# Optimization experiments

Hardware: AMD Instinct MI355X
Metric: run time of the kernel (lower is better)

## Reference

```python
import jax, jax.numpy as jnp
import numpy as np

N = 6            # fixed by nn.Linear(6, h2) after the transpose/squeeze
NEG_SLOPE = 0.01 # F.leaky_relu default


def setup_inputs() -> dict:
    key = jax.random.key(0)
    ks = jax.random.split(key, 12)
    B, H1, H2, H3 = 131072, 64, 512, 256
    in_feat = jax.random.normal(ks[0], (N, B, 1), dtype=jnp.float32)
    # deterministic bidirectional ring: every node has in/out degree 2 (norm='both' safe)
    ar = jnp.arange(N, dtype=jnp.int32)
    src = jnp.concatenate([ar, ar])
    dst = jnp.concatenate([(ar + 1) % N, (ar - 1) % N]).astype(jnp.int32)
    s = 0.2
    W0  = jax.random.normal(ks[1], (1, H1), jnp.float32) * s
    b0  = jax.random.normal(ks[2], (H1,), jnp.float32) * s
    W1  = jax.random.normal(ks[3], (H1, 1), jnp.float32) * s
    b1  = jax.random.normal(ks[4], (1,), jnp.float32) * s
    Wl0 = jax.random.normal(ks[5], (N, H2), jnp.float32) * s
    bl0 = jax.random.normal(ks[6], (H2,), jnp.float32) * s
    Wl2 = jax.random.normal(ks[7], (H2, H3), jnp.float32) * s
    bl2 = jax.random.normal(ks[8], (H3,), jnp.float32) * s
    Wl3 = jax.random.normal(ks[9], (H3, 1), jnp.float32) * s
    bl3 = jax.random.normal(ks[10], (1,), jnp.float32) * s
    return {"in_feat": in_feat, "src": src, "dst": dst,
            "W0": W0, "b0": b0, "W1": W1, "b1": b1,
            "Wl0": Wl0, "bl0": bl0, "Wl2": Wl2, "bl2": bl2,
            "Wl3": Wl3, "bl3": bl3}


def _lrelu(x):
    return jnp.where(x >= 0, x, NEG_SLOPE * x)


def _degree_norms(src, dst):
    ones = jnp.ones(src.shape[0], dtype=jnp.float32)
    deg_out = jax.ops.segment_sum(ones, src, num_segments=N)
    deg_in = jax.ops.segment_sum(ones, dst, num_segments=N)
    return deg_out ** -0.5, deg_in ** -0.5  # DGL GraphConv norm='both'


def _graph_conv(feat, W, b, src, dst, inv_out, inv_in):
    # D_out^{-1/2} A^T D_in^{-1/2} feat  then linear (order is math-equivalent)
    h = feat * inv_out[:, None, None]           # [N,B,F]
    agg = jax.ops.segment_sum(h[src], dst, num_segments=N)  # gather+scatter over edges
    agg = agg * inv_in[:, None, None]
    return agg @ W + b


def reference(in_feat, src, dst, W0, b0, W1, b1, Wl0, bl0, Wl2, bl2, Wl3, bl3):
    inv_out, inv_in = _degree_norms(src, dst)
    h = _lrelu(_graph_conv(in_feat, W0, b0, src, dst, inv_out, inv_in))  # [N,B,h1]
    h = _lrelu(_graph_conv(h, W1, b1, src, dst, inv_out, inv_in))        # [N,B,1]
    x = jnp.transpose(h, (2, 1, 0))[0]   # transpose(0,2).squeeze(0) -> [B,N]
    x = _lrelu(x @ Wl0 + bl0)
    x = _lrelu(x @ Wl2 + bl2)
    x = _lrelu(x @ Wl3 + bl3)            # [B,1]; squeeze(0) is a no-op for B>1
    return x
```

## Files before the change

kernel.cpp:

```cpp
#include <hip/hip_runtime.h>

#define NN   6
#define H1   64
#define H2   512
#define H3   256
#define TM   256
#define KC   32
#define NCH  (H2 / KC)
#define CHUNK_BYTES 32768

typedef short s16x8 __attribute__((ext_vector_type(8)));
typedef float f32x16 __attribute__((ext_vector_type(16)));
typedef float f32x2 __attribute__((ext_vector_type(2)));
typedef unsigned int u32x4 __attribute__((ext_vector_type(4)));

__device__ __forceinline__ unsigned short f2bf(float x) {
    unsigned int u = __float_as_uint(x);
    u += 0x7FFFu + ((u >> 16) & 1u);
    return (unsigned short)(u >> 16);
}
__device__ __forceinline__ float bf2f(unsigned short b) {
    return __uint_as_float(((unsigned int)b) << 16);
}
__device__ __forceinline__ unsigned int cvt_pk_bf16(float a, float b) {
    unsigned int r;
    asm("v_cvt_pk_bf16_f32 %0, %1, %2" : "=v"(r) : "v"(a), "v"(b));
    return r;
}
__device__ __forceinline__ void g2lds16(const void* g, void* l) {
    __builtin_amdgcn_global_load_lds(
        (const __attribute__((address_space(1))) unsigned int*)g,
        (__attribute__((address_space(3))) unsigned int*)l, 16, 0, 0);
}

__global__ void split_w(const float* __restrict__ Wl2,
                        unsigned short* __restrict__ Whl) {
    const int tid = blockIdx.x * 256 + threadIdx.x;
    const int c0 = tid >> 13, q = tid & 8191;
    const int j = q & 7, col = (q >> 3) & 255, th = q >> 11;
    const int k = (c0 << 5) + (th << 3) + j;
    const float w = Wl2[k * H3 + col];
    const unsigned short hi = f2bf(w);
    const unsigned short lo = f2bf(w - bf2f(hi));
    Whl[(c0 << 14) + q] = hi;
    Whl[(c0 << 14) + 8192 + q] = lo;
}

__global__ __launch_bounds__(512, 2)
void gcn_mfma(const float* __restrict__ f,
              const float* __restrict__ W0,
              const float* __restrict__ b0,
              const float* __restrict__ W1,
              const float* __restrict__ b1_,
              const float* __restrict__ Wl0,
              const float* __restrict__ bl0,
              const float* __restrict__ bl2,
              const float* __restrict__ Wl3,
              const float* __restrict__ bl3_,
              const unsigned short* __restrict__ Whl,
              float* __restrict__ out,
              int B)
{
    __shared__ float sW0[H1], sB0[H1], sW1[H1];
    __shared__ float sWl0[NN][H2];
    __shared__ float sBl0[H2];
    __shared__ float sBl2[H3];
    __shared__ float sWl3[H3];
    __shared__ float sF[NN][TM];
    __shared__ float sS[NN][TM];
    __shared__ float sX[NN][TM];
    __shared__ __align__(16) unsigned short sB[2][16384];

    const int t    = threadIdx.x;
    const int lane = t & 63;
    const int w    = t >> 6;
    const int cl   = lane & 31;
    const int h    = lane >> 5;
    const int m0   = blockIdx.x * TM;

    for (int i = t; i < H1; i += 512) { sW0[i] = W0[i]; sB0[i] = b0[i]; sW1[i] = W1[i]; }
    for (int i = t; i < NN * H2; i += 512) sWl0[i >> 9][i & (H2 - 1)] = Wl0[i];
    for (int i = t; i < H2; i += 512) sBl0[i] = bl0[i];
    for (int i = t; i < H3; i += 512) { sBl2[i] = bl2[i]; sWl3[i] = Wl3[i]; }
    for (int i = t; i < NN * TM; i += 512) sF[i >> 8][i & 255] = f[(i >> 8) * B + m0 + (i & 255)];

#define STAGE(CH, BUF) do {                                                        \
        const char* _src = (const char*)Whl + (CH) * CHUNK_BYTES + (w << 12) + (lane << 4); \
        char*       _dst = (char*)&sB[BUF][0] + (w << 12);                         \
        _Pragma("unroll")                                                          \
        for (int _q = 0; _q < 4; ++_q) g2lds16(_src + (_q << 10), _dst + (_q << 10)); \
    } while (0)

    STAGE(0, 0);
    __syncthreads();

    const float b1v = b1_[0];

    for (int v = t; v < NN * TM; v += 512) {
        const int i = v >> 8, r = v & 255;
        const int im = (i + NN - 1) % NN, ip = (i + 1) % NN;
        const float g = 0.5f * (sF[im][r] + sF[ip][r]);
        float s = 0.f;
        #pragma unroll
        for (int c = 0; c < H1; ++c) {
            float hx = g * sW0[c] + sB0[c];
            hx = fmaxf(hx, 0.01f * hx);
            s += hx * sW1[c];
        }
        sS[i][r] = s;
    }
    __syncthreads();
    for (int v = t; v < NN * TM; v += 512) {
        const int i = v >> 8, r = v & 255;
        const int im = (i + NN - 1) % NN, ip = (i + 1) % NN;
        const float xv = 0.5f * (sS[im][r] + sS[ip][r]) + b1v;
        sX[i][r] = fmaxf(xv, 0.01f * xv);
    }
    __syncthreads();

    const int myrow = (w << 5) + cl;
    float xr[NN];
    #pragma unroll
    for (int i = 0; i < NN; ++i) xr[i] = sX[i][myrow];

    f32x16 acc[8];
    #pragma unroll
    for (int c = 0; c < 8; ++c)
        #pragma unroll
        for (int rg = 0; rg < 16; ++rg) acc[c][rg] = 0.f;

#define K0(CH, TT) (((CH) << 5) + ((TT) << 4) + (h << 3))
#define GEN_TT(K0V, AH, AL) do {                                                   \
        const int _k0 = (K0V);                                                     \
        f32x2 _ac[4];                                                              \
        _Pragma("unroll")                                                          \
        for (int _j = 0; _j < 4; ++_j) _ac[_j] = *(const f32x2*)&sBl0[_k0 + 2*_j]; \
        _Pragma("unroll")                                                          \
        for (int _i = 0; _i < 6; ++_i) {                                           \
            const float _xi = xr[_i];                                              \
            _Pragma("unroll")                                                      \
            for (int _j = 0; _j < 4; ++_j)                                         \
                _ac[_j] += _xi * (*(const f32x2*)&sWl0[_i][_k0 + 2*_j]);           \
        }                                                                          \
        unsigned int _hw[4], _lw[4];                                               \
        _Pragma("unroll")                                                          \
        for (int _j = 0; _j < 4; ++_j) {                                           \
            f32x2 _v = _ac[_j];                                                    \
            _v = __builtin_elementwise_max(_v, 0.01f * _v);                        \
            const unsigned int _uh = cvt_pk_bf16(_v[0], _v[1]);                    \
            f32x2 _hf = { __uint_as_float(_uh << 16),                              \
                          __uint_as_float(_uh & 0xFFFF0000u) };                    \
            const f32x2 _r = _v - _hf;                                             \
            _hw[_j] = _uh; _lw[_j] = cvt_pk_bf16(_r[0], _r[1]);                    \
        }                                                                          \
        const u32x4 _u4 = {_hw[0], _hw[1], _hw[2], _hw[3]};                        \
        const u32x4 _l4 = {_lw[0], _lw[1], _lw[2], _lw[3]};                        \
        AH = __builtin_bit_cast(s16x8, _u4);                                       \
        AL = __builtin_bit_cast(s16x8, _l4);                                       \
    } while (0)

#define MFMA_TT(SBC, TT, AH, AL) do {                                              \
        const int _thh = ((TT) << 1) + h;                                          \
        const unsigned short* _bb = &(SBC)[((_thh << 8) + cl) << 3];               \
        _Pragma("unroll")                                                          \
        for (int _g = 0; _g < 2; ++_g) {                                           \
            s16x8 _bh[4];                                                          \
            _Pragma("unroll")                                                      \
            for (int _i = 0; _i < 4; ++_i)                                         \
                _bh[_i] = *(const s16x8*)&_bb[(_g * 4 + _i) << 8];                 \
            _Pragma("unroll")                                                      \
            for (int _i = 0; _i < 4; ++_i)                                         \
                acc[_g*4+_i] = __builtin_amdgcn_mfma_f32_32x32x16_bf16(AH, _bh[_i], acc[_g*4+_i], 0, 0, 0); \
            _Pragma("unroll")                                                      \
            for (int _i = 0; _i < 4; ++_i)                                         \
                acc[_g*4+_i] = __builtin_amdgcn_mfma_f32_32x32x16_bf16(AL, _bh[_i], acc[_g*4+_i], 0, 0, 0); \
            _Pragma("unroll")                                                      \
            for (int _i = 0; _i < 4; ++_i) {                                       \
                const s16x8 _bl = *(const s16x8*)&_bb[8192 + ((_g * 4 + _i) << 8)];\
                acc[_g*4+_i] = __builtin_amdgcn_mfma_f32_32x32x16_bf16(AH, _bl, acc[_g*4+_i], 0, 0, 0); \
            }                                                                      \
        }                                                                          \
    } while (0)

    s16x8 ahA0, alA0, ahA1, alA1;
    s16x8 ahB0, alB0, ahB1, alB1;
    GEN_TT(K0(0, 0), ahA0, alA0);
    GEN_TT(K0(0, 1), ahA1, alA1);

    for (int ch = 0; ch < NCH; ch += 2) {
        STAGE(ch + 1, 1);
        GEN_TT(K0(ch + 1, 0), ahB0, alB0);
        GEN_TT(K0(ch + 1, 1), ahB1, alB1);
        MFMA_TT((&sB[0][0]), 0, ahA0, alA0);
        MFMA_TT((&sB[0][0]), 1, ahA1, alA1);
        __syncthreads();
        if (ch + 2 < NCH) {
            STAGE(ch + 2, 0);
            GEN_TT(K0(ch + 2, 0), ahA0, alA0);
            GEN_TT(K0(ch + 2, 1), ahA1, alA1);
        }
        MFMA_TT((&sB[1][0]), 0, ahB0, alB0);
        MFMA_TT((&sB[1][0]), 1, ahB1, alB1);
        __syncthreads();
    }

    float ps[16];
    #pragma unroll
    for (int rg = 0; rg < 16; ++rg) ps[rg] = 0.f;
    #pragma unroll
    for (int c = 0; c < 8; ++c) {
        const int col = (c << 5) + cl;
        const float b2 = sBl2[col], w3 = sWl3[col];
        #pragma unroll
        for (int rg = 0; rg < 16; ++rg) {
            float v = acc[c][rg] + b2;
            v = fmaxf(v, 0.01f * v);
            ps[rg] += v * w3;
        }
    }
    #pragma unroll
    for (int m = 1; m < 32; m <<= 1)
        #pragma unroll
        for (int rg = 0; rg < 16; ++rg) ps[rg] += __shfl_xor(ps[rg], m);
    if (cl == 0) {
        const float bl3v = bl3_[0];
        #pragma unroll
        for (int rg = 0; rg < 16; ++rg) {
            const int row = (rg & 3) + ((rg >> 2) << 3) + (h << 2);
            const float v = ps[rg] + bl3v;
            out[m0 + (w << 5) + row] = fmaxf(v, 0.01f * v);
        }
    }
}

extern "C" void kernel_launch(void* const* d_in, const int* in_sizes, int n_in,
                              void* d_out, int out_size, void* d_ws, size_t ws_size,
                              hipStream_t stream) {
    const float* f   = (const float*)d_in[0];
    const float* W0  = (const float*)d_in[3];
    const float* b0  = (const float*)d_in[4];
    const float* W1  = (const float*)d_in[5];
    const float* b1  = (const float*)d_in[6];
    const float* Wl0 = (const float*)d_in[7];
    const float* bl0 = (const float*)d_in[8];
    const float* Wl2 = (const float*)d_in[9];
    const float* bl2 = (const float*)d_in[10];
    const float* Wl3 = (const float*)d_in[11];
    const float* bl3 = (const float*)d_in[12];
    float* out = (float*)d_out;
    unsigned short* Whl = (unsigned short*)d_ws;
    const int B = in_sizes[0] / NN;

    split_w<<<dim3(H2 * H3 / 256), 256, 0, stream>>>(Wl2, Whl);
    gcn_mfma<<<dim3(B / TM), 512, 0, stream>>>(f, W0, b0, W1, b1, Wl0, bl0,
                                               bl2, Wl3, bl3, Whl, out, B);
}
```

Baseline: 182.9 us.

## Fuse weight split into kernel with producer/consumer warp specialization

Removes the separate split_w kernel. Four producer waves now stream fp32 Wl2 chunks into LDS, split them into bf16 hi/lo pairs, and build the bf16 A tiles in LDS. The other four consumer waves run only MFMAs on double-buffered LDS tiles. The block tile shrinks from 256 to 128 rows, with the final reduction done through shared memory. This saves one launch and overlaps conversion with matrix math. In exchange, every block redoes the weight split, which is redundant work repeated 1024 times, and only half the waves issue MFMAs.

```diff
diff --git a/kernel.cpp b/kernel.cpp
--- a/kernel.cpp
+++ b/kernel.cpp
@@ -4,24 +4,15 @@
 #define H1   64
 #define H2   512
 #define H3   256
-#define TM   256
-#define KC   32
+#define TM   128
+#define KC   16
 #define NCH  (H2 / KC)
-#define CHUNK_BYTES 32768
 
 typedef short s16x8 __attribute__((ext_vector_type(8)));
 typedef float f32x16 __attribute__((ext_vector_type(16)));
-typedef float f32x2 __attribute__((ext_vector_type(2)));
+typedef float f32x4v __attribute__((ext_vector_type(4)));
 typedef unsigned int u32x4 __attribute__((ext_vector_type(4)));
 
-__device__ __forceinline__ unsigned short f2bf(float x) {
-    unsigned int u = __float_as_uint(x);
-    u += 0x7FFFu + ((u >> 16) & 1u);
-    return (unsigned short)(u >> 16);
-}
-__device__ __forceinline__ float bf2f(unsigned short b) {
-    return __uint_as_float(((unsigned int)b) << 16);
-}
 __device__ __forceinline__ unsigned int cvt_pk_bf16(float a, float b) {
     unsigned int r;
     asm("v_cvt_pk_bf16_f32 %0, %1, %2" : "=v"(r) : "v"(a), "v"(b));
@@ -33,33 +24,20 @@
         (__attribute__((address_space(3))) unsigned int*)l, 16, 0, 0);
 }
 
-__global__ void split_w(const float* __restrict__ Wl2,
-                        unsigned short* __restrict__ Whl) {
-    const int tid = blockIdx.x * 256 + threadIdx.x;
-    const int c0 = tid >> 13, q = tid & 8191;
-    const int j = q & 7, col = (q >> 3) & 255, th = q >> 11;
-    const int k = (c0 << 5) + (th << 3) + j;
-    const float w = Wl2[k * H3 + col];
-    const unsigned short hi = f2bf(w);
-    const unsigned short lo = f2bf(w - bf2f(hi));
-    Whl[(c0 << 14) + q] = hi;
-    Whl[(c0 << 14) + 8192 + q] = lo;
-}
-
 __global__ __launch_bounds__(512, 2)
-void gcn_mfma(const float* __restrict__ f,
-              const float* __restrict__ W0,
-              const float* __restrict__ b0,
-              const float* __restrict__ W1,
-              const float* __restrict__ b1_,
-              const float* __restrict__ Wl0,
-              const float* __restrict__ bl0,
-              const float* __restrict__ bl2,
-              const float* __restrict__ Wl3,
-              const float* __restrict__ bl3_,
-              const unsigned short* __restrict__ Whl,
-              float* __restrict__ out,
-              int B)
+void gcn_fused(const float* __restrict__ f,
+               const float* __restrict__ W0,
+               const float* __restrict__ b0,
+               const float* __restrict__ W1,
+               const float* __restrict__ b1_,
+               const float* __restrict__ Wl0,
+               const float* __restrict__ bl0,
+               const float* __restrict__ Wl2,
+               const float* __restrict__ bl2,
+               const float* __restrict__ Wl3,
+               const float* __restrict__ bl3_,
+               float* __restrict__ out,
+               int B)
 {
     __shared__ float sW0[H1], sB0[H1], sW1[H1];
     __shared__ float sWl0[NN][H2];
@@ -69,7 +47,9 @@
     __shared__ float sF[NN][TM];
     __shared__ float sS[NN][TM];
     __shared__ float sX[NN][TM];
-    __shared__ __align__(16) unsigned short sB[2][16384];
+    __shared__ __align__(16) float sWf[2][4096];
+    __shared__ __align__(16) unsigned short sA[8192];
+    __shared__ __align__(16) unsigned short sB[2][8192];
 
     const int t    = threadIdx.x;
     const int lane = t & 63;
@@ -77,27 +57,28 @@
     const int cl   = lane & 31;
     const int h    = lane >> 5;
     const int m0   = blockIdx.x * TM;
+    const bool prod = (w < 4);
 
     for (int i = t; i < H1; i += 512) { sW0[i] = W0[i]; sB0[i] = b0[i]; sW1[i] = W1[i]; }
     for (int i = t; i < NN * H2; i += 512) sWl0[i >> 9][i & (H2 - 1)] = Wl0[i];
     for (int i = t; i < H2; i += 512) sBl0[i] = bl0[i];
     for (int i = t; i < H3; i += 512) { sBl2[i] = bl2[i]; sWl3[i] = Wl3[i]; }
-    for (int i = t; i < NN * TM; i += 512) sF[i >> 8][i & 255] = f[(i >> 8) * B + m0 + (i & 255)];
-
-#define STAGE(CH, BUF) do {                                                        \
-        const char* _src = (const char*)Whl + (CH) * CHUNK_BYTES + (w << 12) + (lane << 4); \
-        char*       _dst = (char*)&sB[BUF][0] + (w << 12);                         \
-        _Pragma("unroll")                                                          \
-        for (int _q = 0; _q < 4; ++_q) g2lds16(_src + (_q << 10), _dst + (_q << 10)); \
-    } while (0)
-
-    STAGE(0, 0);
+    for (int i = t; i < NN * TM; i += 512) sF[i >> 7][i & (TM - 1)] = f[(i >> 7) * B + m0 + (i & (TM - 1))];
+
+#define STAGE_WF(CH, BUF) do {                                                     \
+        const char* _s = (const char*)Wl2 + (CH) * 16384 + (w << 12) + (lane << 4);\
+        char*       _d = (char*)&sWf[BUF][0] + (w << 12);                          \
+        _Pragma("unroll")                                                          \
+        for (int _q = 0; _q < 4; ++_q) g2lds16(_s + (_q << 10), _d + (_q << 10));  \
+    } while (0)
+
+    if (prod) { STAGE_WF(0, 0); STAGE_WF(1, 1); }
     __syncthreads();
 
     const float b1v = b1_[0];
 
     for (int v = t; v < NN * TM; v += 512) {
-        const int i = v >> 8, r = v & 255;
+        const int i = v >> 7, r = v & (TM - 1);
         const int im = (i + NN - 1) % NN, ip = (i + 1) % NN;
         const float g = 0.5f * (sF[im][r] + sF[ip][r]);
         float s = 0.f;
@@ -111,125 +92,178 @@
     }
     __syncthreads();
     for (int v = t; v < NN * TM; v += 512) {
-        const int i = v >> 8, r = v & 255;
+        const int i = v >> 7, r = v & (TM - 1);
         const int im = (i + NN - 1) % NN, ip = (i + 1) % NN;
         const float xv = 0.5f * (sS[im][r] + sS[ip][r]) + b1v;
         sX[i][r] = fmaxf(xv, 0.01f * xv);
     }
     __syncthreads();
 
-    const int myrow = (w << 5) + cl;
+#define SPLIT_W(SRCBUF, DSTBUF) do {                                               \
+        const int _col = (w << 6) + lane;                                          \
+        _Pragma("unroll")                                                          \
+        for (int _o = 0; _o < 2; ++_o) {                                           \
+            float _v[8];                                                           \
+            _Pragma("unroll")                                                      \
+            for (int _j = 0; _j < 8; ++_j)                                         \
+                _v[_j] = sWf[SRCBUF][(((_o << 3) + _j) << 8) + _col];              \
+            unsigned int _hi[4], _lo[4];                                           \
+            _Pragma("unroll")                                                      \
+            for (int _p = 0; _p < 4; ++_p) {                                       \
+                const unsigned int _uh = cvt_pk_bf16(_v[2*_p], _v[2*_p+1]);        \
+                const float _h0 = __uint_as_float(_uh << 16);                      \
+                const float _h1 = __uint_as_float(_uh & 0xFFFF0000u);              \
+                _hi[_p] = _uh;                                                     \
+                _lo[_p] = cvt_pk_bf16(_v[2*_p] - _h0, _v[2*_p+1] - _h1);           \
+            }                                                                      \
+            *(u32x4*)&sB[DSTBUF][(_o << 11) + (_col << 3)] =                       \
+                (u32x4){_hi[0], _hi[1], _hi[2], _hi[3]};                           \
+            *(u32x4*)&sB[DSTBUF][4096 + (_o << 11) + (_col << 3)] =                \
+                (u32x4){_lo[0], _lo[1], _lo[2], _lo[3]};                           \
+        }                                                                          \
+    } while (0)
+
+#define GEN_A(CH, BUF) do {                                                        \
+        const int _k0 = ((CH) << 4) + (poct << 3);                                 \
+        f32x4v _za = *(const f32x4v*)&sBl0[_k0];                                   \
+        f32x4v _zb = *(const f32x4v*)&sBl0[_k0 + 4];                               \
+        _Pragma("unroll")                                                          \
+        for (int _i = 0; _i < 6; ++_i) {                                           \
+            const f32x4v _wa = *(const f32x4v*)&sWl0[_i][_k0];                     \
+            const f32x4v _wb = *(const f32x4v*)&sWl0[_i][_k0 + 4];                 \
+            _za += xr[_i] * _wa;                                                   \
+            _zb += xr[_i] * _wb;                                                   \
+        }                                                                          \
+        _za = __builtin_elementwise_max(_za, 0.01f * _za);                         \
+        _zb = __builtin_elementwise_max(_zb, 0.01f * _zb);                         \
+        const float _vv[8] = {_za[0],_za[1],_za[2],_za[3],_zb[0],_zb[1],_zb[2],_zb[3]}; \
+        unsigned int _hi[4], _lo[4];                                               \
+        _Pragma("unroll")                                                          \
+        for (int _p = 0; _p < 4; ++_p) {                                           \
+            const unsigned int _uh = cvt_pk_bf16(_vv[2*_p], _vv[2*_p+1]);          \
+            const float _h0 = __uint_as_float(_uh << 16);                          \
+            const float _h1 = __uint_as_float(_uh & 0xFFFF0000u);                  \
+            _hi[_p] = _uh;                                                         \
+            _lo[_p] = cvt_pk_bf16(_vv[2*_p] - _h0, _vv[2*_p+1] - _h1);             \
+        }                                                                          \
+        *(u32x4*)&sA[((((BUF) << 2) + poct) << 10) + (prow << 3)] =                \
+            (u32x4){_hi[0], _hi[1], _hi[2], _hi[3]};                               \
+        *(u32x4*)&sA[((((BUF) << 2) + 2 + poct) << 10) + (prow << 3)] =            \
+            (u32x4){_lo[0], _lo[1], _lo[2], _lo[3]};                               \
+    } while (0)
+
+#define CONS_WIN(BUF) do {                                                         \
+        s16x8 _ah[4], _al[4], _bh[2], _bl[2];                                      \
+        const int _ab = ((((BUF) << 2) + h) << 10) + (cl << 3);                    \
+        _Pragma("unroll")                                                          \
+        for (int _rt = 0; _rt < 4; ++_rt) {                                        \
+            _ah[_rt] = *(const s16x8*)&sA[_ab + (_rt << 8)];                       \
+            _al[_rt] = *(const s16x8*)&sA[_ab + 2048 + (_rt << 8)];                \
+        }                                                                          \
+        const int _bb = (h << 11) + (((wc2 << 6) + cl) << 3);                      \
+        _Pragma("unroll")                                                          \
+        for (int _g = 0; _g < 2; ++_g) {                                           \
+            _bh[_g] = *(const s16x8*)&sB[BUF][_bb + (_g << 8)];                    \
+            _bl[_g] = *(const s16x8*)&sB[BUF][4096 + _bb + (_g << 8)];             \
+        }                                                                          \
+        _Pragma("unroll")                                                          \
+        for (int _rt = 0; _rt < 4; ++_rt)                                          \
+            _Pragma("unroll")                                                      \
+            for (int _g = 0; _g < 2; ++_g)                                         \
+                acc[_rt][_g] = __builtin_amdgcn_mfma_f32_32x32x16_bf16(_ah[_rt], _bh[_g], acc[_rt][_g], 0, 0, 0); \
+        _Pragma("unroll")                                                          \
+        for (int _rt = 0; _rt < 4; ++_rt)                                          \
+            _Pragma("unroll")                                                      \
+            for (int _g = 0; _g < 2; ++_g)                                         \
+                acc[_rt][_g] = __builtin_amdgcn_mfma_f32_32x32x16_bf16(_al[_rt], _bh[_g], acc[_rt][_g], 0, 0, 0); \
+        _Pragma("unroll")                                                          \
+        for (int _rt = 0; _rt < 4; ++_rt)                                          \
+            _Pragma("unroll")                                                      \
+            for (int _g = 0; _g < 2; ++_g)                                         \
+                acc[_rt][_g] = __builtin_amdgcn_mfma_f32_32x32x16_bf16(_ah[_rt], _bl[_g], acc[_rt][_g], 0, 0, 0); \
+    } while (0)
+
     float xr[NN];
-    #pragma unroll
-    for (int i = 0; i < NN; ++i) xr[i] = sX[i][myrow];
-
-    f32x16 acc[8];
-    #pragma unroll
-    for (int c = 0; c < 8; ++c)
-        #pragma unroll
-        for (int rg = 0; rg < 16; ++rg) acc[c][rg] = 0.f;
-
-#define K0(CH, TT) (((CH) << 5) + ((TT) << 4) + (h << 3))
-#define GEN_TT(K0V, AH, AL) do {                                                   \
-        const int _k0 = (K0V);                                                     \
-        f32x2 _ac[4];                                                              \
-        _Pragma("unroll")                                                          \
-        for (int _j = 0; _j < 4; ++_j) _ac[_j] = *(const f32x2*)&sBl0[_k0 + 2*_j]; \
-        _Pragma("unroll")                                                          \
-        for (int _i = 0; _i < 6; ++_i) {                                           \
-            const float _xi = xr[_i];                                              \
-            _Pragma("unroll")                                                      \
-            for (int _j = 0; _j < 4; ++_j)                                         \
-                _ac[_j] += _xi * (*(const f32x2*)&sWl0[_i][_k0 + 2*_j]);           \
-        }                                                                          \
-        unsigned int _hw[4], _lw[4];                                               \
-        _Pragma("unroll")                                                          \
-        for (int _j = 0; _j < 4; ++_j) {                                           \
-            f32x2 _v = _ac[_j];                                                    \
-            _v = __builtin_elementwise_max(_v, 0.01f * _v);                        \
-            const unsigned int _uh = cvt_pk_bf16(_v[0], _v[1]);                    \
-            f32x2 _hf = { __uint_as_float(_uh << 16),                              \
-                          __uint_as_float(_uh & 0xFFFF0000u) };                    \
-            const f32x2 _r = _v - _hf;                                             \
-            _hw[_j] = _uh; _lw[_j] = cvt_pk_bf16(_r[0], _r[1]);                    \
-        }                                                                          \
-        const u32x4 _u4 = {_hw[0], _hw[1], _hw[2], _hw[3]};                        \
-        const u32x4 _l4 = {_lw[0], _lw[1], _lw[2], _lw[3]};                        \
-        AH = __builtin_bit_cast(s16x8, _u4);                                       \
-        AL = __builtin_bit_cast(s16x8, _l4);                                       \
-    } while (0)
-
-#define MFMA_TT(SBC, TT, AH, AL) do {                                              \
-        const int _thh = ((TT) << 1) + h;                                          \
-        const unsigned short* _bb = &(SBC)[((_thh << 8) + cl) << 3];               \
-        _Pragma("unroll")                                                          \
-        for (int _g = 0; _g < 2; ++_g) {                                           \
-            s16x8 _bh[4];                                                          \
-            _Pragma("unroll")                                                      \
-            for (int _i = 0; _i < 4; ++_i)                                         \
-                _bh[_i] = *(const s16x8*)&_bb[(_g * 4 + _i) << 8];                 \
-            _Pragma("unroll")                                                      \
-            for (int _i = 0; _i < 4; ++_i)                                         \
-                acc[_g*4+_i] = __builtin_amdgcn_mfma_f32_32x32x16_bf16(AH, _bh[_i], acc[_g*4+_i], 0, 0, 0); \
-            _Pragma("unroll")                                                      \
-            for (int _i = 0; _i < 4; ++_i)                                         \
-                acc[_g*4+_i] = __builtin_amdgcn_mfma_f32_32x32x16_bf16(AL, _bh[_i], acc[_g*4+_i], 0, 0, 0); \
-            _Pragma("unroll")                                                      \
-            for (int _i = 0; _i < 4; ++_i) {                                       \
-                const s16x8 _bl = *(const s16x8*)&_bb[8192 + ((_g * 4 + _i) << 8)];\
-                acc[_g*4+_i] = __builtin_amdgcn_mfma_f32_32x32x16_bf16(AH, _bl, acc[_g*4+_i], 0, 0, 0); \
-            }                                                                      \
-        }                                                                          \
-    } while (0)
-
-    s16x8 ahA0, alA0, ahA1, alA1;
-    s16x8 ahB0, alB0, ahB1, alB1;
-    GEN_TT(K0(0, 0), ahA0, alA0);
-    GEN_TT(K0(0, 1), ahA1, alA1);
+    int poct = 0, prow = 0, wc2 = 0;
+    f32x16 acc[4][2];
+
+    if (prod) {
+        poct = w >> 1;
+        prow = ((w & 1) << 6) + lane;
+        #pragma unroll
+        for (int i = 0; i < NN; ++i) xr[i] = sX[i][prow];
+        SPLIT_W(0, 0);
+        GEN_A(0, 0);
+    } else {
+        wc2 = w - 4;
+        #pragma unroll
+        for (int rt = 0; rt < 4; ++rt)
+            #pragma unroll
+            for (int g = 0; g < 2; ++g)
+                #pragma unroll
+                for (int rg = 0; rg < 16; ++rg) acc[rt][g][rg] = 0.f;
+    }
+    __syncthreads();
 
     for (int ch = 0; ch < NCH; ch += 2) {
-        STAGE(ch + 1, 1);
-        GEN_TT(K0(ch + 1, 0), ahB0, alB0);
-        GEN_TT(K0(ch + 1, 1), ahB1, alB1);
-        MFMA_TT((&sB[0][0]), 0, ahA0, alA0);
-        MFMA_TT((&sB[0][0]), 1, ahA1, alA1);
+        if (prod) {
+            if (ch + 2 < NCH) STAGE_WF(ch + 2, 0);
+            SPLIT_W(1, 1);
+            GEN_A(ch + 1, 1);
+        } else {
+            CONS_WIN(0);
+        }
         __syncthreads();
-        if (ch + 2 < NCH) {
-            STAGE(ch + 2, 0);
-            GEN_TT(K0(ch + 2, 0), ahA0, alA0);
-            GEN_TT(K0(ch + 2, 1), ahA1, alA1);
-        }
-        MFMA_TT((&sB[1][0]), 0, ahB0, alB0);
-        MFMA_TT((&sB[1][0]), 1, ahB1, alB1);
+        if (prod) {
+            if (ch + 3 < NCH) STAGE_WF(ch + 3, 1);
+            if (ch + 2 < NCH) { SPLIT_W(0, 0); GEN_A(ch + 2, 0); }
+        } else {
+            CONS_WIN(1);
+        }
         __syncthreads();
     }
 
-    float ps[16];
-    #pragma unroll
-    for (int rg = 0; rg < 16; ++rg) ps[rg] = 0.f;
-    #pragma unroll
-    for (int c = 0; c < 8; ++c) {
-        const int col = (c << 5) + cl;
-        const float b2 = sBl2[col], w3 = sWl3[col];
-        #pragma unroll
-        for (int rg = 0; rg < 16; ++rg) {
-            float v = acc[c][rg] + b2;
-            v = fmaxf(v, 0.01f * v);
-            ps[rg] += v * w3;
-        }
-    }
-    #pragma unroll
-    for (int m = 1; m < 32; m <<= 1)
-        #pragma unroll
-        for (int rg = 0; rg < 16; ++rg) ps[rg] += __shfl_xor(ps[rg], m);
-    if (cl == 0) {
+    float* sRed = &sF[0][0];
+    if (!prod) {
+        float ps[4][16];
+        #pragma unroll
+        for (int rt = 0; rt < 4; ++rt)
+            #pragma unroll
+            for (int rg = 0; rg < 16; ++rg) ps[rt][rg] = 0.f;
+        #pragma unroll
+        for (int g = 0; g < 2; ++g) {
+            const int col = (wc2 << 6) + (g << 5) + cl;
+            const float b2 = sBl2[col], w3 = sWl3[col];
+            #pragma unroll
+            for (int rt = 0; rt < 4; ++rt)
+                #pragma unroll
+                for (int rg = 0; rg < 16; ++rg) {
+                    float v = acc[rt][g][rg] + b2;
+                    v = fmaxf(v, 0.01f * v);
+                    ps[rt][rg] += v * w3;
+                }
+        }
+        #pragma unroll
+        for (int msk = 1; msk < 32; msk <<= 1)
+            #pragma unroll
+            for (int rt = 0; rt < 4; ++rt)
+                #pragma unroll
+                for (int rg = 0; rg < 16; ++rg) ps[rt][rg] += __shfl_xor(ps[rt][rg], msk);
+        if (cl == 0) {
+            #pragma unroll
+            for (int rt = 0; rt < 4; ++rt)
+                #pragma unroll
+                for (int rg = 0; rg < 16; ++rg) {
+                    const int row = (rt << 5) + (rg & 3) + ((rg >> 2) << 3) + (h << 2);
+                    sRed[(wc2 << 7) + row] = ps[rt][rg];
+                }
+        }
+    }
+    __syncthreads();
+    if (t < TM) {
         const float bl3v = bl3_[0];
-        #pragma unroll
-        for (int rg = 0; rg < 16; ++rg) {
-            const int row = (rg & 3) + ((rg >> 2) << 3) + (h << 2);
-            const float v = ps[rg] + bl3v;
-            out[m0 + (w << 5) + row] = fmaxf(v, 0.01f * v);
-        }
+        const float v = sRed[t] + sRed[TM + t] + sRed[2 * TM + t] + sRed[3 * TM + t] + bl3v;
+        out[m0 + t] = fmaxf(v, 0.01f * v);
     }
 }
 
@@ -248,10 +282,8 @@
     const float* Wl3 = (const float*)d_in[11];
     const float* bl3 = (const float*)d_in[12];
     float* out = (float*)d_out;
-    unsigned short* Whl = (unsigned short*)d_ws;
     const int B = in_sizes[0] / NN;
 
-    split_w<<<dim3(H2 * H3 / 256), 256, 0, stream>>>(Wl2, Whl);
-    gcn_mfma<<<dim3(B / TM), 512, 0, stream>>>(f, W0, b0, W1, b1, Wl0, bl0,
-                                               bl2, Wl3, bl3, Whl, out, B);
-}
+    gcn_fused<<<dim3(B / TM), 512, 0, stream>>>(f, W0, b0, W1, b1, Wl0, bl0,
+                                                Wl2, bl2, Wl3, bl3, out, B);
+}
```

After: 252.5 us. +38.0%, slower.
